# Performance work log

Hardware: AMD Instinct MI355X
Metric: run time of the kernel (lower is better)

## Reference

```python
import jax, jax.numpy as jnp
import numpy as np

NEG = -9e15
ALPHA = 0.2  # leaky relu negative slope


def setup_inputs() -> dict:
    key = jax.random.key(0)
    k1, k2, k3, k4 = jax.random.split(key, 4)
    B, N, d = 8, 2048, 128
    h = jax.random.normal(k1, (B, N, d), dtype=jnp.float32)
    adj = jax.random.randint(k2, (B, N, N), 0, 2, dtype=jnp.int32)
    W = jax.random.normal(k3, (d, d), dtype=jnp.float32) * (1.414 / np.sqrt(d))
    a = jax.random.normal(k4, (2 * d, 1), dtype=jnp.float32) * 0.1
    return {"h": h, "adj": adj, "W": W, "a": a}


def reference(h, adj, W, a):
    d = W.shape[1]
    Wh = jnp.matmul(h, W)                       # [B, N, d]  (dropout p=0 -> identity)
    Wh1 = jnp.matmul(Wh, a[:d])                 # [B, N, 1]
    Wh2 = jnp.matmul(Wh, a[d:])                 # [B, N, 1]
    e = jax.nn.leaky_relu(Wh1 + jnp.swapaxes(Wh2, 1, 2), negative_slope=ALPHA)  # [B, N, N]
    scores = jnp.where(adj > 0, e, NEG)
    attention = jax.nn.softmax(scores, axis=-1)  # [B, N, N]
    h_prime = jnp.matmul(attention, Wh)          # [B, N, d]
    out = h + h_prime                            # residual=True, concat=False
    return out, attention
```

## Files before the change

kernel.cpp:

```cpp
#include <hip/hip_runtime.h>
#include <cstdint>
#include <cstddef>

typedef float  v4f __attribute__((ext_vector_type(4)));
typedef short  v8s __attribute__((ext_vector_type(8)));
typedef int    v4i __attribute__((ext_vector_type(4)));
typedef unsigned int v2u __attribute__((ext_vector_type(2)));

#define BB 8
#define NN 2048
#define DD 128
#define TI 16
#define NEGV (-9e15f)

__device__ __forceinline__ unsigned short f2bf(float x) {
  unsigned u = __float_as_uint(x);
  u = u + 0x7FFFu + ((u >> 16) & 1u);
  return (unsigned short)(u >> 16);
}

__global__ __launch_bounds__(256) void gat_k1(
    const float* __restrict__ h, const float* __restrict__ W, const float* __restrict__ a,
    short* __restrict__ whbT, float* __restrict__ wh1g, float* __restrict__ wh2g)
{
  __shared__ __align__(16) unsigned short wT[DD * 136];
  __shared__ __align__(16) unsigned short staging[DD * 72];

  const int tid  = threadIdx.x;
  const int lane = tid & 63;
  const int wid  = tid >> 6;
  const int m16  = lane & 15;
  const int quad = lane >> 4;
  const int b    = blockIdx.y;
  const int i0   = blockIdx.x * 64;

  {
    const v4f* W4 = (const v4f*)W;
    #pragma unroll
    for (int it = 0; it < 16; it++) {
      int idx = it * 256 + tid;
      int k  = idx >> 5;
      int c4 = (idx & 31) * 4;
      v4f wv = W4[idx];
      #pragma unroll
      for (int q = 0; q < 4; q++)
        wT[(c4 + q) * 136 + k] = f2bf(wv[q]);
    }
  }

  const float* hrow = h + (size_t)(b * NN + i0 + wid * 16 + m16) * DD;
  v8s af[4];
  #pragma unroll
  for (int ks = 0; ks < 4; ks++) {
    v4f x0 = *(const v4f*)(hrow + ks * 32 + quad * 8);
    v4f x1 = *(const v4f*)(hrow + ks * 32 + quad * 8 + 4);
    v8s t;
    t[0] = (short)f2bf(x0.x); t[1] = (short)f2bf(x0.y);
    t[2] = (short)f2bf(x0.z); t[3] = (short)f2bf(x0.w);
    t[4] = (short)f2bf(x1.x); t[5] = (short)f2bf(x1.y);
    t[6] = (short)f2bf(x1.z); t[7] = (short)f2bf(x1.w);
    af[ks] = t;
  }
  __syncthreads();

  v4f acc[8];
  #pragma unroll
  for (int t = 0; t < 8; t++) acc[t] = (v4f){0.f, 0.f, 0.f, 0.f};

  #pragma unroll
  for (int ks = 0; ks < 4; ks++) {
    #pragma unroll
    for (int t = 0; t < 8; t++) {
      v8s bf = *(const v8s*)&wT[(t * 16 + m16) * 136 + ks * 32 + quad * 8];
      acc[t] = __builtin_amdgcn_mfma_f32_16x16x32_bf16(af[ks], bf, acc[t], 0, 0, 0);
    }
  }

  {
    float a1v[8], a2v[8];
    #pragma unroll
    for (int t = 0; t < 8; t++) {
      a1v[t] = a[t * 16 + m16];
      a2v[t] = a[DD + t * 16 + m16];
    }
    #pragma unroll
    for (int r = 0; r < 4; r++) {
      float p1 = 0.f, p2 = 0.f;
      #pragma unroll
      for (int t = 0; t < 8; t++) {
        p1 += acc[t][r] * a1v[t];
        p2 += acc[t][r] * a2v[t];
      }
      #pragma unroll
      for (int off = 8; off > 0; off >>= 1) {
        p1 += __shfl_xor(p1, off);
        p2 += __shfl_xor(p2, off);
      }
      if (m16 == 0) {
        int gi = b * NN + i0 + wid * 16 + quad * 4 + r;
        wh1g[gi] = p1;
        wh2g[gi] = p2;
      }
    }
  }

  #pragma unroll
  for (int t = 0; t < 8; t++)
    #pragma unroll
    for (int r = 0; r < 4; r++)
      staging[(t * 16 + m16) * 72 + wid * 16 + quad * 4 + r] = f2bf(acc[t][r]);
  __syncthreads();

  #pragma unroll
  for (int it = 0; it < 4; it++) {
    int idx = it * 256 + tid;
    int c  = idx >> 3;
    int i8 = idx & 7;
    v8s val = *(const v8s*)&staging[c * 72 + i8 * 8];
    *(v8s*)(whbT + (size_t)b * DD * NN + (size_t)c * NN + i0 + i8 * 8) = val;
  }
}

__global__ __launch_bounds__(256) void gat_k2(
    const float* __restrict__ h, const int* __restrict__ adj,
    const short* __restrict__ whbT, const float* __restrict__ wh1g,
    const float* __restrict__ wh2g, float* __restrict__ out,
    float* __restrict__ attout)
{
  __shared__ __align__(16) float wh2s[NN];
  __shared__ float wh1s[TI];
  __shared__ unsigned int maskw[TI * 64];
  __shared__ float m_s[TI];
  __shared__ float rs_s[TI];
  __shared__ __align__(16) unsigned short atile[2][TI * 72];

  const int tid = threadIdx.x;
  const int lane = tid & 63;
  const int wid = tid >> 6;
  const int b = blockIdx.y;
  const int i0 = blockIdx.x * TI;

  {
    const v4f* w2g4 = (const v4f*)(wh2g + (size_t)b * NN);
    ((v4f*)wh2s)[tid] = w2g4[tid];
    ((v4f*)wh2s)[tid + 256] = w2g4[tid + 256];
  }
  if (tid < TI) wh1s[tid] = wh1g[b * NN + i0 + tid];
  __syncthreads();

  for (int ii = wid; ii < TI; ii += 4) {
    const v4i* arow = (const v4i*)(adj + (size_t)(b * NN + i0 + ii) * NN);
    const float wh1v = wh1s[ii];
    float e[32];
    float m = -INFINITY;
    unsigned mbits = 0u;
    #pragma unroll
    for (int u = 0; u < 8; u++) {
      v4i av = __builtin_nontemporal_load(&arow[u * 64 + lane]);
      v4f w2v = ((const v4f*)wh2s)[u * 64 + lane];
      #pragma unroll
      for (int q = 0; q < 4; q++) {
        bool mk = av[q] > 0;
        float x = wh1v + w2v[q];
        float ev = mk ? (x > 0.f ? x : 0.2f * x) : NEGV;
        e[u * 4 + q] = ev;
        m = fmaxf(m, ev);
        mbits |= (mk ? 1u : 0u) << (u * 4 + q);
      }
    }
    maskw[ii * 64 + lane] = mbits;
    #pragma unroll
    for (int off = 32; off > 0; off >>= 1) m = fmaxf(m, __shfl_xor(m, off));
    float s = 0.f;
    #pragma unroll
    for (int k = 0; k < 32; k++) s += __expf(e[k] - m);
    #pragma unroll
    for (int off = 32; off > 0; off >>= 1) s += __shfl_xor(s, off);
    if (lane == 0) { m_s[ii] = m; rs_s[ii] = 1.f / s; }
  }
  __syncthreads();

  float* attrow_base = attout + (size_t)(b * NN + i0) * NN;
  const short* whbT_b = whbT + (size_t)b * DD * NN;
  const int m16 = lane & 15;
  const int quad = lane >> 4;
  const int irow = tid >> 4;
  const int jq = tid & 15;
  const float wh1v = wh1s[irow];
  const float mi_r = m_s[irow];
  const float rsi_r = rs_s[irow];

  v4f acc[2];
  acc[0] = (v4f){0.f, 0.f, 0.f, 0.f};
  acc[1] = (v4f){0.f, 0.f, 0.f, 0.f};

  for (int jc = 0; jc < 32; jc++) {
    const int j0 = jc * 64;
    const int ubit = (jc >> 2) << 2;
    unsigned short* buf = atile[jc & 1];

    {
      unsigned mw = maskw[irow * 64 + ((jc * 16 + jq) & 63)];
      v4f w2v = ((const v4f*)wh2s)[(j0 >> 2) + jq];
      v4f av;
      unsigned short ab[4];
      #pragma unroll
      for (int q = 0; q < 4; q++) {
        float x = wh1v + w2v[q];
        float ev = ((mw >> (ubit + q)) & 1u) ? (x > 0.f ? x : 0.2f * x) : NEGV;
        float at = __expf(ev - mi_r) * rsi_r;
        av[q] = at;
        ab[q] = f2bf(at);
      }
      __builtin_nontemporal_store(av, (v4f*)(attrow_base + (size_t)irow * NN + j0 + jq * 4));
      v2u uv;
      uv[0] = (unsigned)ab[0] | ((unsigned)ab[1] << 16);
      uv[1] = (unsigned)ab[2] | ((unsigned)ab[3] << 16);
      *(v2u*)&buf[irow * 72 + jq * 4] = uv;
    }

    v8s bfr[2][2];
    #pragma unroll
    for (int ks = 0; ks < 2; ks++)
      #pragma unroll
      for (int t = 0; t < 2; t++)
        bfr[ks][t] = *(const v8s*)(whbT_b + (size_t)((wid * 2 + t) * 16 + m16) * NN
                                   + j0 + ks * 32 + quad * 8);

    __syncthreads();

    #pragma unroll
    for (int ks = 0; ks < 2; ks++) {
      v8s af = *(const v8s*)&buf[m16 * 72 + ks * 32 + quad * 8];
      acc[0] = __builtin_amdgcn_mfma_f32_16x16x32_bf16(af, bfr[ks][0], acc[0], 0, 0, 0);
      acc[1] = __builtin_amdgcn_mfma_f32_16x16x32_bf16(af, bfr[ks][1], acc[1], 0, 0, 0);
    }
  }

  #pragma unroll
  for (int t = 0; t < 2; t++) {
    #pragma unroll
    for (int r = 0; r < 4; r++) {
      size_t gidx = ((size_t)(b * NN + i0 + quad * 4 + r)) * DD + (wid * 2 + t) * 16 + m16;
      out[gidx] = h[gidx] + acc[t][r];
    }
  }
}

extern "C" void kernel_launch(void* const* d_in, const int* in_sizes, int n_in,
                              void* d_out, int out_size, void* d_ws, size_t ws_size,
                              hipStream_t stream) {
  const float* h  = (const float*)d_in[0];
  const int* adj  = (const int*)d_in[1];
  const float* W  = (const float*)d_in[2];
  const float* a  = (const float*)d_in[3];

  float* out    = (float*)d_out;
  float* attout = out + (size_t)BB * NN * DD;

  short* whbT = (short*)d_ws;
  float* wh1  = (float*)((char*)d_ws + (size_t)BB * DD * NN * 2);
  float* wh2  = wh1 + BB * NN;

  gat_k1<<<dim3(NN / 64, BB), 256, 0, stream>>>(h, W, a, whbT, wh1, wh2);
  gat_k2<<<dim3(NN / TI, BB), 256, 0, stream>>>(h, adj, whbT, wh1, wh2, out, attout);
}
```

Measured before the change: 285.9 us.

## Compute attention fragments per wave in registers, removing LDS tile and barriers

Each wave now recomputes the bf16 attention A-fragment for its MFMAs directly in registers from the mask bits, wh2 and row stats. This removes the shared attention tile and the per-chunk __syncthreads, and processes 128 columns per iteration. The cost is that the exp and leaky-relu work is duplicated four times across waves, with only one wave per k-slice writing the fp32 attention output. The mask rows are padded to 66 words, and launch bounds request 4 blocks per CU.

```diff
diff --git a/kernel.cpp b/kernel.cpp
--- a/kernel.cpp
+++ b/kernel.cpp
@@ -121,7 +121,7 @@
   }
 }
 
-__global__ __launch_bounds__(256) void gat_k2(
+__global__ __launch_bounds__(256, 4) void gat_k2(
     const float* __restrict__ h, const int* __restrict__ adj,
     const short* __restrict__ whbT, const float* __restrict__ wh1g,
     const float* __restrict__ wh2g, float* __restrict__ out,
@@ -129,10 +129,9 @@
 {
   __shared__ __align__(16) float wh2s[NN];
   __shared__ float wh1s[TI];
-  __shared__ unsigned int maskw[TI * 64];
+  __shared__ __align__(8) unsigned int maskw[TI * 66];
   __shared__ float m_s[TI];
   __shared__ float rs_s[TI];
-  __shared__ __align__(16) unsigned short atile[2][TI * 72];
 
   const int tid = threadIdx.x;
   const int lane = tid & 63;
@@ -168,7 +167,7 @@
         mbits |= (mk ? 1u : 0u) << (u * 4 + q);
       }
     }
-    maskw[ii * 64 + lane] = mbits;
+    maskw[ii * 66 + lane] = mbits;
     #pragma unroll
     for (int off = 32; off > 0; off >>= 1) m = fmaxf(m, __shfl_xor(m, off));
     float s = 0.f;
@@ -180,60 +179,73 @@
   }
   __syncthreads();
 
-  float* attrow_base = attout + (size_t)(b * NN + i0) * NN;
   const short* whbT_b = whbT + (size_t)b * DD * NN;
   const int m16 = lane & 15;
   const int quad = lane >> 4;
-  const int irow = tid >> 4;
-  const int jq = tid & 15;
-  const float wh1v = wh1s[irow];
-  const float mi_r = m_s[irow];
-  const float rsi_r = rs_s[irow];
+  const float wh1v = wh1s[m16];
+  const float mi_r = m_s[m16];
+  const float rsi_r = rs_s[m16];
+  const unsigned int* mrow = &maskw[m16 * 66];
+  float* attrow = attout + (size_t)(b * NN + i0 + m16) * NN;
+  const short* bb0 = whbT_b + (size_t)((wid * 2 + 0) * 16 + m16) * NN;
+  const short* bb1 = whbT_b + (size_t)((wid * 2 + 1) * 16 + m16) * NN;
 
   v4f acc[2];
   acc[0] = (v4f){0.f, 0.f, 0.f, 0.f};
   acc[1] = (v4f){0.f, 0.f, 0.f, 0.f};
 
-  for (int jc = 0; jc < 32; jc++) {
-    const int j0 = jc * 64;
-    const int ubit = (jc >> 2) << 2;
-    unsigned short* buf = atile[jc & 1];
-
-    {
-      unsigned mw = maskw[irow * 64 + ((jc * 16 + jq) & 63)];
-      v4f w2v = ((const v4f*)wh2s)[(j0 >> 2) + jq];
-      v4f av;
-      unsigned short ab[4];
+  for (int jc = 0; jc < 16; jc++) {
+    const int j0 = jc * 128;
+    const unsigned U4 = (unsigned)((j0 >> 8) << 2);
+
+    v8s bfr[4][2];
+    #pragma unroll
+    for (int ks = 0; ks < 4; ks++) {
+      bfr[ks][0] = *(const v8s*)(bb0 + j0 + ks * 32 + quad * 8);
+      bfr[ks][1] = *(const v8s*)(bb1 + j0 + ks * 32 + quad * 8);
+    }
+
+    v8s af[4];
+    #pragma unroll
+    for (int ks = 0; ks < 4; ks++) {
+      const int jbase = j0 + ks * 32 + quad * 8;
+      v4f w2a = *(const v4f*)&wh2s[jbase];
+      v4f w2b = *(const v4f*)&wh2s[jbase + 4];
+      v2u mwv = *(const v2u*)&mrow[(jbase >> 2) & 63];
+      unsigned nib0 = (mwv[0] >> U4) & 0xFu;
+      unsigned nib1 = (mwv[1] >> U4) & 0xFu;
+      v4f av0, av1;
+      unsigned short ab[8];
       #pragma unroll
       for (int q = 0; q < 4; q++) {
-        float x = wh1v + w2v[q];
-        float ev = ((mw >> (ubit + q)) & 1u) ? (x > 0.f ? x : 0.2f * x) : NEGV;
+        float x = wh1v + w2a[q];
+        float ev = ((nib0 >> q) & 1u) ? (x > 0.f ? x : 0.2f * x) : NEGV;
         float at = __expf(ev - mi_r) * rsi_r;
-        av[q] = at;
+        av0[q] = at;
         ab[q] = f2bf(at);
       }
-      __builtin_nontemporal_store(av, (v4f*)(attrow_base + (size_t)irow * NN + j0 + jq * 4));
-      v2u uv;
-      uv[0] = (unsigned)ab[0] | ((unsigned)ab[1] << 16);
-      uv[1] = (unsigned)ab[2] | ((unsigned)ab[3] << 16);
-      *(v2u*)&buf[irow * 72 + jq * 4] = uv;
-    }
-
-    v8s bfr[2][2];
-    #pragma unroll
-    for (int ks = 0; ks < 2; ks++)
-      #pragma unroll
-      for (int t = 0; t < 2; t++)
-        bfr[ks][t] = *(const v8s*)(whbT_b + (size_t)((wid * 2 + t) * 16 + m16) * NN
-                                   + j0 + ks * 32 + quad * 8);
-
-    __syncthreads();
-
-    #pragma unroll
-    for (int ks = 0; ks < 2; ks++) {
-      v8s af = *(const v8s*)&buf[m16 * 72 + ks * 32 + quad * 8];
-      acc[0] = __builtin_amdgcn_mfma_f32_16x16x32_bf16(af, bfr[ks][0], acc[0], 0, 0, 0);
-      acc[1] = __builtin_amdgcn_mfma_f32_16x16x32_bf16(af, bfr[ks][1], acc[1], 0, 0, 0);
+      #pragma unroll
+      for (int q = 0; q < 4; q++) {
+        float x = wh1v + w2b[q];
+        float ev = ((nib1 >> q) & 1u) ? (x > 0.f ? x : 0.2f * x) : NEGV;
+        float at = __expf(ev - mi_r) * rsi_r;
+        av1[q] = at;
+        ab[4 + q] = f2bf(at);
+      }
+      if (ks == wid) {
+        __builtin_nontemporal_store(av0, (v4f*)(attrow + jbase));
+        __builtin_nontemporal_store(av1, (v4f*)(attrow + jbase + 4));
+      }
+      v8s t;
+      #pragma unroll
+      for (int q = 0; q < 8; q++) t[q] = (short)ab[q];
+      af[ks] = t;
+    }
+
+    #pragma unroll
+    for (int ks = 0; ks < 4; ks++) {
+      acc[0] = __builtin_amdgcn_mfma_f32_16x16x32_bf16(af[ks], bfr[ks][0], acc[0], 0, 0, 0);
+      acc[1] = __builtin_amdgcn_mfma_f32_16x16x32_bf16(af[ks], bfr[ks][1], acc[1], 0, 0, 0);
     }
   }
 
```

Result: no change. 290.7 us (+1.7%).

## Widen attention/PV chunk to 256 columns with vectorized stores and fewer barriers

Applied to the files above, without the earlier changes.

The second loop now processes 256 columns per iteration instead of 64. Each thread computes 16 contiguous attention values, emits wider nontemporal stores, and packs bf16 pairs with the intrinsic converter. The mask words are padded and read as vectors, and each barrier is followed by 8 MFMA k-steps instead of 2. This is meant to cut synchronization overhead and raise memory-level parallelism, at the cost of a larger LDS tile and more register pressure under an occupancy hint.

```diff
diff --git a/kernel.cpp b/kernel.cpp
--- a/kernel.cpp
+++ b/kernel.cpp
@@ -1,4 +1,5 @@
 #include <hip/hip_runtime.h>
+#include <hip/hip_bf16.h>
 #include <cstdint>
 #include <cstddef>
 
@@ -6,6 +7,7 @@
 typedef short  v8s __attribute__((ext_vector_type(8)));
 typedef int    v4i __attribute__((ext_vector_type(4)));
 typedef unsigned int v2u __attribute__((ext_vector_type(2)));
+typedef unsigned int v4u __attribute__((ext_vector_type(4)));
 
 #define BB 8
 #define NN 2048
@@ -17,6 +19,12 @@
   unsigned u = __float_as_uint(x);
   u = u + 0x7FFFu + ((u >> 16) & 1u);
   return (unsigned short)(u >> 16);
+}
+
+__device__ __forceinline__ unsigned pack_bf2(float lo, float hi) {
+  __hip_bfloat162 p = __float22bfloat162_rn(make_float2(lo, hi));
+  unsigned u; __builtin_memcpy(&u, &p, 4);
+  return u;
 }
 
 __global__ __launch_bounds__(256) void gat_k1(
@@ -121,7 +129,7 @@
   }
 }
 
-__global__ __launch_bounds__(256) void gat_k2(
+__global__ __launch_bounds__(256, 4) void gat_k2(
     const float* __restrict__ h, const int* __restrict__ adj,
     const short* __restrict__ whbT, const float* __restrict__ wh1g,
     const float* __restrict__ wh2g, float* __restrict__ out,
@@ -129,10 +137,10 @@
 {
   __shared__ __align__(16) float wh2s[NN];
   __shared__ float wh1s[TI];
-  __shared__ unsigned int maskw[TI * 64];
+  __shared__ __align__(16) unsigned int maskw[TI * 68];
   __shared__ float m_s[TI];
   __shared__ float rs_s[TI];
-  __shared__ __align__(16) unsigned short atile[2][TI * 72];
+  __shared__ __align__(16) unsigned short atile[2][TI * 264];
 
   const int tid = threadIdx.x;
   const int lane = tid & 63;
@@ -168,7 +176,7 @@
         mbits |= (mk ? 1u : 0u) << (u * 4 + q);
       }
     }
-    maskw[ii * 64 + lane] = mbits;
+    maskw[ii * 68 + lane] = mbits;
     #pragma unroll
     for (int off = 32; off > 0; off >>= 1) m = fmaxf(m, __shfl_xor(m, off));
     float s = 0.f;
@@ -180,7 +188,6 @@
   }
   __syncthreads();
 
-  float* attrow_base = attout + (size_t)(b * NN + i0) * NN;
   const short* whbT_b = whbT + (size_t)b * DD * NN;
   const int m16 = lane & 15;
   const int quad = lane >> 4;
@@ -189,51 +196,52 @@
   const float wh1v = wh1s[irow];
   const float mi_r = m_s[irow];
   const float rsi_r = rs_s[irow];
+  float* attrow = attout + (size_t)(b * NN + i0 + irow) * NN;
+  const short* bb0 = whbT_b + (size_t)((wid * 2 + 0) * 16 + m16) * NN;
+  const short* bb1 = whbT_b + (size_t)((wid * 2 + 1) * 16 + m16) * NN;
 
   v4f acc[2];
   acc[0] = (v4f){0.f, 0.f, 0.f, 0.f};
   acc[1] = (v4f){0.f, 0.f, 0.f, 0.f};
 
-  for (int jc = 0; jc < 32; jc++) {
-    const int j0 = jc * 64;
-    const int ubit = (jc >> 2) << 2;
+  for (int jc = 0; jc < 8; jc++) {
+    const int j0 = jc * 256;
     unsigned short* buf = atile[jc & 1];
 
-    {
-      unsigned mw = maskw[irow * 64 + ((jc * 16 + jq) & 63)];
-      v4f w2v = ((const v4f*)wh2s)[(j0 >> 2) + jq];
-      v4f av;
-      unsigned short ab[4];
+    v4u mw4 = *(const v4u*)&maskw[irow * 68 + jq * 4];
+    const unsigned sh = (unsigned)(jc * 4);
+
+    unsigned pk[8];
+    #pragma unroll
+    for (int u = 0; u < 4; u++) {
+      v4f w2v = *(const v4f*)&wh2s[j0 + jq * 16 + u * 4];
+      unsigned nib = (mw4[u] >> sh) & 0xFu;
+      v4f o;
       #pragma unroll
       for (int q = 0; q < 4; q++) {
         float x = wh1v + w2v[q];
-        float ev = ((mw >> (ubit + q)) & 1u) ? (x > 0.f ? x : 0.2f * x) : NEGV;
-        float at = __expf(ev - mi_r) * rsi_r;
-        av[q] = at;
-        ab[q] = f2bf(at);
-      }
-      __builtin_nontemporal_store(av, (v4f*)(attrow_base + (size_t)irow * NN + j0 + jq * 4));
-      v2u uv;
-      uv[0] = (unsigned)ab[0] | ((unsigned)ab[1] << 16);
-      uv[1] = (unsigned)ab[2] | ((unsigned)ab[3] << 16);
-      *(v2u*)&buf[irow * 72 + jq * 4] = uv;
-    }
-
-    v8s bfr[2][2];
-    #pragma unroll
-    for (int ks = 0; ks < 2; ks++)
-      #pragma unroll
-      for (int t = 0; t < 2; t++)
-        bfr[ks][t] = *(const v8s*)(whbT_b + (size_t)((wid * 2 + t) * 16 + m16) * NN
-                                   + j0 + ks * 32 + quad * 8);
-
+        float ev = ((nib >> q) & 1u) ? (x > 0.f ? x : 0.2f * x) : NEGV;
+        o[q] = __expf(ev - mi_r) * rsi_r;
+      }
+      __builtin_nontemporal_store(o, (v4f*)(attrow + j0 + jq * 16 + u * 4));
+      pk[u * 2 + 0] = pack_bf2(o[0], o[1]);
+      pk[u * 2 + 1] = pack_bf2(o[2], o[3]);
+    }
+    {
+      v4u w0 = (v4u){pk[0], pk[1], pk[2], pk[3]};
+      v4u w1 = (v4u){pk[4], pk[5], pk[6], pk[7]};
+      *(v4u*)&buf[irow * 264 + jq * 16] = w0;
+      *(v4u*)&buf[irow * 264 + jq * 16 + 8] = w1;
+    }
     __syncthreads();
 
     #pragma unroll
-    for (int ks = 0; ks < 2; ks++) {
-      v8s af = *(const v8s*)&buf[m16 * 72 + ks * 32 + quad * 8];
-      acc[0] = __builtin_amdgcn_mfma_f32_16x16x32_bf16(af, bfr[ks][0], acc[0], 0, 0, 0);
-      acc[1] = __builtin_amdgcn_mfma_f32_16x16x32_bf16(af, bfr[ks][1], acc[1], 0, 0, 0);
+    for (int ks = 0; ks < 8; ks++) {
+      v8s af = *(const v8s*)&buf[m16 * 264 + ks * 32 + quad * 8];
+      v8s b0 = *(const v8s*)(bb0 + j0 + ks * 32 + quad * 8);
+      v8s b1 = *(const v8s*)(bb1 + j0 + ks * 32 + quad * 8);
+      acc[0] = __builtin_amdgcn_mfma_f32_16x16x32_bf16(af, b0, acc[0], 0, 0, 0);
+      acc[1] = __builtin_amdgcn_mfma_f32_16x16x32_bf16(af, b1, acc[1], 0, 0, 0);
     }
   }
 
```

New measurement: 396.1 us. +38.6%, slower.
